# Kernel tuning notes

Measured on AMD Instinct MI355X. Metric: run time of the kernel, lower is better.

## Reference

```python
import jax, jax.numpy as jnp
import numpy as np

HIDDEN = 2048
HEAD = 256
VDIM = 512  # double_v_dim=True -> 2*head_size
GAMMA = 0.96875
SCALE_BASE = 512.0  # xpos default


def _rotate_every_two(x):
    # (x0, x1, x2, x3, ...) -> (-x1, x0, -x3, x2, ...)
    x1 = x[..., ::2]
    x2 = x[..., 1::2]
    return jnp.stack((-x2, x1), axis=-1).reshape(x.shape)


def _xpos(x, downscale=False, offset=0):
    # Standard XPOS (rotary + exponential scaling) as used in RetNet repos.
    S, d = x.shape[1], x.shape[2]
    d2 = d // 2
    scale_vec = (jnp.arange(0, d, 2, dtype=jnp.float32) + 0.4 * d) / (1.4 * d)  # [d2]
    pos = jnp.arange(S + offset, dtype=jnp.float32)
    scale = scale_vec[None, :] ** (pos[:, None] / SCALE_BASE)  # [S+off, d2]
    inv_freq = 1.0 / (10000.0 ** (jnp.arange(d2, dtype=jnp.float32) / d2))
    sinusoid = pos[:, None] * inv_freq[None, :]  # [S+off, d2]
    sin, cos = jnp.sin(sinusoid), jnp.cos(sinusoid)
    scale, sin, cos = scale[-S:], sin[-S:], cos[-S:]
    if downscale:
        scale = 1.0 / scale
    sin_s = jnp.repeat(sin * scale, 2, axis=-1)  # duplicate_interleave -> [S, d]
    cos_s = jnp.repeat(cos * scale, 2, axis=-1)
    return x * cos_s[None] + _rotate_every_two(x) * sin_s[None]


def _decay_matrix(S):
    # D[n, m] = gamma^(n-m) for n >= m else 0 (NaN/overflow-safe)
    n = jnp.arange(S, dtype=jnp.float32)
    diff = n[:, None] - n[None, :]
    mask = diff >= 0
    return jnp.where(mask, GAMMA ** jnp.where(mask, diff, 0.0), 0.0)


def setup_inputs() -> dict:
    key = jax.random.key(0)
    k1, k2, k3, k4 = jax.random.split(key, 4)
    B, S = 4, 4096
    X = jax.random.normal(k1, (B, S, HIDDEN), dtype=jnp.float32)
    W_Q = jax.random.normal(k2, (HIDDEN, HEAD), dtype=jnp.float32) / HIDDEN
    W_K = jax.random.normal(k3, (HIDDEN, HEAD), dtype=jnp.float32) / HIDDEN
    W_V = jax.random.normal(k4, (HIDDEN, VDIM), dtype=jnp.float32) / HIDDEN
    return {"X": X, "W_Q": W_Q, "W_K": W_K, "W_V": W_V}


def reference(X, W_Q, W_K, W_V):
    S = X.shape[1]
    Q = _xpos(X @ W_Q)                      # [B, S, HEAD]
    K = _xpos(X @ W_K, downscale=True)      # [B, S, HEAD]
    V = X @ W_V                             # [B, S, VDIM]
    D = _decay_matrix(S)                    # [S, S]
    retention = jnp.einsum('bqd,bkd->bqk', Q, K) * D[None]  # [B, S, S]
    return retention @ V                    # [B, S, VDIM]
```

## Files before the change

### kernel.cpp

```cpp
#include <hip/hip_runtime.h>
#include <math.h>

#define NB 4
#define SEQ 4096
#define HID 2048
#define DH 256
#define DV 512
#define NQKV 1024
#define CHUNK 128
#define NCH 32
#define MROWS (NB * SEQ)
#define LOG2_GAMMA (-0.045803689613124794f)
#define LOG2_10000 13.287712379549449f

typedef __attribute__((ext_vector_type(8))) short short8;
typedef __attribute__((ext_vector_type(4))) float floatx4;

__device__ __forceinline__ unsigned short bf16_rne(float v) {
    unsigned int u = __float_as_uint(v);
    u += 0x7fff + ((u >> 16) & 1);
    return (unsigned short)(u >> 16);
}
__device__ __forceinline__ float b2f(unsigned short h) {
    return __uint_as_float((unsigned int)h << 16);
}

__device__ __forceinline__ void gld16(const void* g, void* l) {
    __builtin_amdgcn_global_load_lds(
        reinterpret_cast<const __attribute__((address_space(1))) unsigned int*>(
            reinterpret_cast<uintptr_t>(g)),
        reinterpret_cast<__attribute__((address_space(3))) unsigned int*>(
            reinterpret_cast<uintptr_t>(l)),
        16, 0, 0);
}

__global__ __launch_bounds__(256) void xcvt_kernel(
    const float* __restrict__ X, unsigned short* __restrict__ Xb)
{
    const int i = blockIdx.x * 256 + threadIdx.x;
    float4 x = ((const float4*)X)[i];
    ushort4 h;
    h.x = bf16_rne(x.x); h.y = bf16_rne(x.y);
    h.z = bf16_rne(x.z); h.w = bf16_rne(x.w);
    ((ushort4*)Xb)[i] = h;
}

__global__ __launch_bounds__(256) void wcvt_kernel(
    const float* __restrict__ WQ, const float* __restrict__ WK,
    const float* __restrict__ WV, unsigned short* __restrict__ Bt)
{
    __shared__ unsigned short sh[64][65];
    const int bid = blockIdx.x;
    const int kt = bid & 31;
    const int ntile = bid >> 5;
    const int k0 = kt * 64, n0 = ntile * 64;

    const float* W; int ld, nl0;
    if (n0 < 256)      { W = WQ; ld = DH; nl0 = n0; }
    else if (n0 < 512) { W = WK; ld = DH; nl0 = n0 - 256; }
    else               { W = WV; ld = DV; nl0 = n0 - 512; }

    const int t = threadIdx.x;
#pragma unroll
    for (int p = 0; p < 4; p++) {
        const int kl = (t >> 4) + p * 16;
        const int ng = (t & 15) * 4;
        float4 w = *(const float4*)&W[(size_t)(k0 + kl) * ld + nl0 + ng];
        sh[kl][ng + 0] = bf16_rne(w.x);
        sh[kl][ng + 1] = bf16_rne(w.y);
        sh[kl][ng + 2] = bf16_rne(w.z);
        sh[kl][ng + 3] = bf16_rne(w.w);
    }
    __syncthreads();
#pragma unroll
    for (int p = 0; p < 4; p++) {
        const int nl = (t >> 4) + p * 16;
        const int kg = (t & 15) * 4;
        ushort4 h;
        h.x = sh[kg + 0][nl]; h.y = sh[kg + 1][nl];
        h.z = sh[kg + 2][nl]; h.w = sh[kg + 3][nl];
        *(ushort4*)&Bt[(size_t)(n0 + nl) * HID + k0 + kg] = h;
    }
}

__global__ __launch_bounds__(512, 1) void qkv_mfma_kernel(
    const unsigned short* __restrict__ Xb, const unsigned short* __restrict__ Bt,
    unsigned short* __restrict__ Qb, unsigned short* __restrict__ Kb,
    unsigned short* __restrict__ Vb, unsigned short* __restrict__ Vt)
{
    __shared__ unsigned short Ah[128 * 32];
    __shared__ unsigned short Bh[128 * 32];

    const int bid = blockIdx.x;
    const int xcd = bid & 7;
    const int nt  = (bid >> 3) & 7;
    const int mt  = (xcd << 4) | (bid >> 6);
    const int m0 = mt * 128, n0 = nt * 128;

    const int t = threadIdx.x;
    const int w = t >> 6, lane = t & 63;
    const int wm = (w & 1) << 6;
    const int wn = (w >> 1) << 5;

    floatx4 acc[4][2];
#pragma unroll
    for (int i = 0; i < 4; i++)
#pragma unroll
        for (int j = 0; j < 2; j++) acc[i][j] = (floatx4)0.0f;

    const int srow = lane >> 2, scol = (lane & 3) * 8;
    const size_t aoff = (size_t)(m0 + w * 16 + srow) * HID + scol;
    const size_t boff = (size_t)(n0 + w * 16 + srow) * HID + scol;
    unsigned short* const ldsA = &Ah[(w * 16) * 32];
    unsigned short* const ldsB = &Bh[(w * 16) * 32];

    const int fr = lane & 15, fq = (lane >> 4) * 8;

    for (int k0 = 0; k0 < HID; k0 += 32) {
        __syncthreads();
        gld16(Xb + aoff + k0, ldsA);
        gld16(Bt + boff + k0, ldsB);
        __syncthreads();

        short8 ah[4], bh[2];
#pragma unroll
        for (int i = 0; i < 4; i++)
            ah[i] = *(const short8*)&Ah[(wm + i * 16 + fr) * 32 + fq];
#pragma unroll
        for (int j = 0; j < 2; j++)
            bh[j] = *(const short8*)&Bh[(wn + j * 16 + fr) * 32 + fq];
#pragma unroll
        for (int i = 0; i < 4; i++)
#pragma unroll
            for (int j = 0; j < 2; j++)
                acc[i][j] = __builtin_amdgcn_mfma_f32_16x16x32_bf16(ah[i], bh[j], acc[i][j], 0, 0, 0);
    }

    const int cl = lane & 15, rq = (lane >> 4) << 2;
    if (n0 >= 512) {
#pragma unroll
        for (int i = 0; i < 4; i++)
#pragma unroll
            for (int j = 0; j < 2; j++) {
                const int c = n0 - 512 + wn + j * 16 + cl;
#pragma unroll
                for (int r = 0; r < 4; r++) {
                    const int m = m0 + wm + i * 16 + rq + r;
                    const unsigned short hv = bf16_rne(acc[i][j][r]);
                    Vb[(size_t)m * DV + c] = hv;
                    Vt[(size_t)c * MROWS + m] = hv;
                }
            }
    } else {
        unsigned short* dst = (n0 < 256) ? Qb : Kb;
        const float sgn = (n0 < 256) ? 1.f : -1.f;
        const int nb = (n0 < 256) ? n0 : n0 - 256;
#pragma unroll
        for (int j = 0; j < 2; j++) {
            const int c = nb + wn + j * 16 + cl;
            const float jj = (float)(c >> 1);
            const float sv = (2.f * jj + 0.4f * 256.f) * (1.f / (1.4f * 256.f));
            const float l2sv = __log2f(sv) * sgn * (1.f / 512.f);
            const float invf = exp2f(jj * (-LOG2_10000 / 128.f));
            const bool odd = (c & 1) != 0;
#pragma unroll
            for (int i = 0; i < 4; i++) {
#pragma unroll
                for (int r = 0; r < 4; r++) {
                    const int m = m0 + wm + i * 16 + rq + r;
                    const float s = (float)(m & (SEQ - 1));
                    const float x = acc[i][j][r];
                    const float p = __shfl_xor(x, 1, 64);
                    const float sc = exp2f(s * l2sv);
                    const float ang = s * invf;
                    const float sn = __sinf(ang), cs = __cosf(ang);
                    const float o = odd ? sc * (x * cs + p * sn)
                                        : sc * (x * cs - p * sn);
                    dst[(size_t)m * DH + c] = bf16_rne(o);
                }
            }
        }
    }
}

__global__ __launch_bounds__(256, 1) void chunk_kv_kernel(
    const unsigned short* __restrict__ Kb, const unsigned short* __restrict__ Vb,
    float* __restrict__ Ut)
{
    __shared__ float kls[32][68];
    __shared__ float vls[32][132];

    const int bid = blockIdx.x;
    const int vq = bid & 3;
    const int ht = (bid >> 2) & 3;
    const int c  = (bid >> 4) & 31;
    const int b  = bid >> 9;
    const int dh0 = ht * 64, dv0 = vq * 128;
    const int t = threadIdx.x, tx = t & 15, ty = t >> 4;

    float acc[4][8];
#pragma unroll
    for (int i = 0; i < 4; i++)
#pragma unroll
        for (int j = 0; j < 8; j++) acc[i][j] = 0.f;

    const int klr = t >> 4, klc = (t & 15) << 2;
    const int vlr = t >> 5, vlc = (t & 31) << 2;

    for (int i0 = 0; i0 < CHUNK; i0 += 32) {
        __syncthreads();
#pragma unroll
        for (int p = 0; p < 2; p++) {
            const int il = klr + 16 * p;
            const int i = i0 + il;
            const int row = b * SEQ + c * CHUNK + i;
            const float wgt = exp2f((float)(CHUNK - i) * LOG2_GAMMA);
            ushort4 kq = *(const ushort4*)&Kb[(size_t)row * DH + dh0 + klc];
            kls[il][klc + 0] = b2f(kq.x) * wgt;
            kls[il][klc + 1] = b2f(kq.y) * wgt;
            kls[il][klc + 2] = b2f(kq.z) * wgt;
            kls[il][klc + 3] = b2f(kq.w) * wgt;
        }
#pragma unroll
        for (int p = 0; p < 4; p++) {
            const int il = vlr + 8 * p;
            const int row = b * SEQ + c * CHUNK + i0 + il;
            ushort4 vv = *(const ushort4*)&Vb[(size_t)row * DV + dv0 + vlc];
            vls[il][vlc + 0] = b2f(vv.x);
            vls[il][vlc + 1] = b2f(vv.y);
            vls[il][vlc + 2] = b2f(vv.z);
            vls[il][vlc + 3] = b2f(vv.w);
        }
        __syncthreads();
#pragma unroll
        for (int i = 0; i < 32; i++) {
            float af[4], bf[8];
            *(float4*)&af[0] = *(const float4*)&kls[i][ty * 4];
            *(float4*)&bf[0] = *(const float4*)&vls[i][tx * 8];
            *(float4*)&bf[4] = *(const float4*)&vls[i][tx * 8 + 4];
#pragma unroll
            for (int ii = 0; ii < 4; ii++)
#pragma unroll
                for (int jj = 0; jj < 8; jj++) acc[ii][jj] += af[ii] * bf[jj];
        }
    }

#pragma unroll
    for (int jj = 0; jj < 8; jj++) {
        const int dv = dv0 + tx * 8 + jj;
        const size_t base = ((size_t)(b * NCH + c) * DV + dv) * DH + dh0 + ty * 4;
        *(float4*)&Ut[base] = make_float4(acc[0][jj], acc[1][jj], acc[2][jj], acc[3][jj]);
    }
}

__global__ __launch_bounds__(256) void scan_kernel(float* __restrict__ Ut)
{
    const int t = blockIdx.x * 256 + threadIdx.x;
    const int b = t >> 17;
    const int r = t & 131071;
    const float gC = exp2f((float)CHUNK * LOG2_GAMMA);
    float s = 0.f;
    const size_t base = (size_t)b * NCH * 131072 + r;
    for (int c = 0; c < NCH; c++) {
        const size_t off = base + (size_t)c * 131072;
        const float u = Ut[off];
        Ut[off] = s;
        s = gC * s + u;
    }
}

__global__ __launch_bounds__(512, 1) void out_mfma_kernel(
    const unsigned short* __restrict__ Qb, const unsigned short* __restrict__ Kb,
    const unsigned short* __restrict__ Vt, const float* __restrict__ St,
    float* __restrict__ out)
{
    __shared__ unsigned short Pa[128 * 136];
    __shared__ unsigned short As[128 * 32];
    __shared__ unsigned short Bs[128 * 32];

    const int bid = blockIdx.x;
    const int vq = bid & 3;
    const int c  = (bid >> 2) & 31;
    const int b  = bid >> 7;
    const int dv0 = vq * 128;
    const int row0 = b * SEQ + c * CHUNK;

    const int t = threadIdx.x;
    const int w = t >> 6, lane = t & 63;
    const int wm = (w & 1) << 6;
    const int wn = (w >> 1) << 5;
    const int fr = lane & 15, fq = (lane >> 4) * 8;
    const int cl = lane & 15, rq = (lane >> 4) << 2;
    const int srow = lane >> 2, scol = (lane & 3) * 8;

    floatx4 acc[4][2];
#pragma unroll
    for (int i = 0; i < 4; i++)
#pragma unroll
        for (int j = 0; j < 2; j++) acc[i][j] = (floatx4)0.0f;

    for (int d0 = 0; d0 < DH; d0 += 32) {
        __syncthreads();
        gld16(&Qb[(size_t)(row0 + w * 16 + srow) * DH + d0 + scol], &As[(w * 16) * 32]);
        gld16(&Kb[(size_t)(row0 + w * 16 + srow) * DH + d0 + scol], &Bs[(w * 16) * 32]);
        __syncthreads();
        short8 a[4], bb[2];
#pragma unroll
        for (int i = 0; i < 4; i++)
            a[i] = *(const short8*)&As[(wm + i * 16 + fr) * 32 + fq];
#pragma unroll
        for (int j = 0; j < 2; j++)
            bb[j] = *(const short8*)&Bs[(wn + j * 16 + fr) * 32 + fq];
#pragma unroll
        for (int i = 0; i < 4; i++)
#pragma unroll
            for (int j = 0; j < 2; j++)
                acc[i][j] = __builtin_amdgcn_mfma_f32_16x16x32_bf16(a[i], bb[j], acc[i][j], 0, 0, 0);
    }

#pragma unroll
    for (int i = 0; i < 4; i++)
#pragma unroll
        for (int j = 0; j < 2; j++) {
            const int jj = wn + j * 16 + cl;
#pragma unroll
            for (int r = 0; r < 4; r++) {
                const int ii = wm + i * 16 + rq + r;
                const int diff = ii - jj;
                const float v = (diff >= 0) ? acc[i][j][r] * exp2f((float)diff * LOG2_GAMMA) : 0.f;
                Pa[ii * 136 + jj] = bf16_rne(v);
            }
            acc[i][j] = (floatx4)0.0f;
        }

    for (int k0 = 0; k0 < CHUNK; k0 += 32) {
        __syncthreads();
        gld16(&Vt[(size_t)(dv0 + w * 16 + srow) * MROWS + row0 + k0 + scol], &Bs[(w * 16) * 32]);
        __syncthreads();
        short8 a[4], bb[2];
#pragma unroll
        for (int i = 0; i < 4; i++)
            a[i] = *(const short8*)&Pa[(wm + i * 16 + fr) * 136 + k0 + fq];
#pragma unroll
        for (int j = 0; j < 2; j++)
            bb[j] = *(const short8*)&Bs[(wn + j * 16 + fr) * 32 + fq];
#pragma unroll
        for (int i = 0; i < 4; i++)
#pragma unroll
            for (int j = 0; j < 2; j++)
                acc[i][j] = __builtin_amdgcn_mfma_f32_16x16x32_bf16(a[i], bb[j], acc[i][j], 0, 0, 0);
    }

    const size_t stbase = ((size_t)(b * NCH + c) * DV + dv0) * DH;
    const int xr = t >> 2, xc = (t & 3) * 8;
    const float gx = exp2f((float)xr * LOG2_GAMMA);
    for (int d0 = 0; d0 < DH; d0 += 32) {
        __syncthreads();
        {
            ushort4 q0 = *(const ushort4*)&Qb[(size_t)(row0 + xr) * DH + d0 + xc];
            ushort4 q1 = *(const ushort4*)&Qb[(size_t)(row0 + xr) * DH + d0 + xc + 4];
            ushort4 h0, h1;
            h0.x = bf16_rne(b2f(q0.x) * gx); h0.y = bf16_rne(b2f(q0.y) * gx);
            h0.z = bf16_rne(b2f(q0.z) * gx); h0.w = bf16_rne(b2f(q0.w) * gx);
            h1.x = bf16_rne(b2f(q1.x) * gx); h1.y = bf16_rne(b2f(q1.y) * gx);
            h1.z = bf16_rne(b2f(q1.z) * gx); h1.w = bf16_rne(b2f(q1.w) * gx);
            *(ushort4*)&As[xr * 32 + xc] = h0;
            *(ushort4*)&As[xr * 32 + xc + 4] = h1;
        }
        {
            float4 s0 = *(const float4*)&St[stbase + (size_t)xr * DH + d0 + xc];
            float4 s1 = *(const float4*)&St[stbase + (size_t)xr * DH + d0 + xc + 4];
            ushort4 h0, h1;
            h0.x = bf16_rne(s0.x); h0.y = bf16_rne(s0.y);
            h0.z = bf16_rne(s0.z); h0.w = bf16_rne(s0.w);
            h1.x = bf16_rne(s1.x); h1.y = bf16_rne(s1.y);
            h1.z = bf16_rne(s1.z); h1.w = bf16_rne(s1.w);
            *(ushort4*)&Bs[xr * 32 + xc] = h0;
            *(ushort4*)&Bs[xr * 32 + xc + 4] = h1;
        }
        __syncthreads();
        short8 a[4], bb[2];
#pragma unroll
        for (int i = 0; i < 4; i++)
            a[i] = *(const short8*)&As[(wm + i * 16 + fr) * 32 + fq];
#pragma unroll
        for (int j = 0; j < 2; j++)
            bb[j] = *(const short8*)&Bs[(wn + j * 16 + fr) * 32 + fq];
#pragma unroll
        for (int i = 0; i < 4; i++)
#pragma unroll
            for (int j = 0; j < 2; j++)
                acc[i][j] = __builtin_amdgcn_mfma_f32_16x16x32_bf16(a[i], bb[j], acc[i][j], 0, 0, 0);
    }

#pragma unroll
    for (int i = 0; i < 4; i++)
#pragma unroll
        for (int j = 0; j < 2; j++) {
            const int dv = dv0 + wn + j * 16 + cl;
#pragma unroll
            for (int r = 0; r < 4; r++) {
                const int m = row0 + wm + i * 16 + rq + r;
                out[(size_t)m * DV + dv] = acc[i][j][r];
            }
        }
}

extern "C" void kernel_launch(void* const* d_in, const int* in_sizes, int n_in,
                              void* d_out, int out_size, void* d_ws, size_t ws_size,
                              hipStream_t stream) {
    const float* X  = (const float*)d_in[0];
    const float* WQ = (const float*)d_in[1];
    const float* WK = (const float*)d_in[2];
    const float* WV = (const float*)d_in[3];
    float* out = (float*)d_out;

    char* ws = (char*)d_ws;
    unsigned short* Qb = (unsigned short*)ws;
    unsigned short* Kb = Qb + (size_t)MROWS * DH;
    unsigned short* Vb = Kb + (size_t)MROWS * DH;
    unsigned short* Vt = Vb + (size_t)MROWS * DV;
    float*          Ut = (float*)(Vt + (size_t)MROWS * DV);
    unsigned short* Xb = (unsigned short*)Ut;
    unsigned short* Bt = (unsigned short*)(Ut + (size_t)NB * NCH * DV * DH);

    xcvt_kernel<<<(MROWS * HID / 4) / 256, 256, 0, stream>>>(X, Xb);
    wcvt_kernel<<<512, 256, 0, stream>>>(WQ, WK, WV, Bt);
    qkv_mfma_kernel<<<1024, 512, 0, stream>>>(Xb, Bt, Qb, Kb, Vb, Vt);
    chunk_kv_kernel<<<2048, 256, 0, stream>>>(Kb, Vb, Ut);
    scan_kernel<<<2048, 256, 0, stream>>>(Ut);
    out_mfma_kernel<<<512, 512, 0, stream>>>(Qb, Kb, Vt, Ut, out);
}
```

Baseline: 414.6 us.

## Move chunk KV state to MFMA, store bf16 states, double K-step per barrier

The per-chunk K^T·V state computation moves from scalar FP32 FMAs to bf16 MFMA. It reads transposed K and V buffers that the QKV kernel now writes directly, which drops the row-major V copy. The scan writes bf16 states so the output kernel can load them asynchronously instead of converting fp32 on the fly. The GEMM loops in the QKV and output kernels stage two 32-wide K slices per barrier pair to halve synchronisations. The costs are extra strided transposed K writes, more LDS use, and bf16 rounding of the weighted K values and the states.

```diff
diff --git a/kernel.cpp b/kernel.cpp
--- a/kernel.cpp
+++ b/kernel.cpp
@@ -10,6 +10,8 @@
 #define CHUNK 128
 #define NCH 32
 #define MROWS (NB * SEQ)
+#define GAMMA 0.96875f
+#define GAMMA_INV 1.0322580645161290f
 #define LOG2_GAMMA (-0.045803689613124794f)
 #define LOG2_10000 13.287712379549449f
 
@@ -86,10 +88,10 @@
 __global__ __launch_bounds__(512, 1) void qkv_mfma_kernel(
     const unsigned short* __restrict__ Xb, const unsigned short* __restrict__ Bt,
     unsigned short* __restrict__ Qb, unsigned short* __restrict__ Kb,
-    unsigned short* __restrict__ Vb, unsigned short* __restrict__ Vt)
-{
-    __shared__ unsigned short Ah[128 * 32];
-    __shared__ unsigned short Bh[128 * 32];
+    unsigned short* __restrict__ Kt, unsigned short* __restrict__ Vt)
+{
+    __shared__ unsigned short Ah[2 * 128 * 32];
+    __shared__ unsigned short Bh[2 * 128 * 32];
 
     const int bid = blockIdx.x;
     const int xcd = bid & 7;
@@ -111,29 +113,36 @@
     const int srow = lane >> 2, scol = (lane & 3) * 8;
     const size_t aoff = (size_t)(m0 + w * 16 + srow) * HID + scol;
     const size_t boff = (size_t)(n0 + w * 16 + srow) * HID + scol;
-    unsigned short* const ldsA = &Ah[(w * 16) * 32];
-    unsigned short* const ldsB = &Bh[(w * 16) * 32];
+    unsigned short* const ldsA0 = &Ah[(w * 16) * 32];
+    unsigned short* const ldsA1 = &Ah[4096 + (w * 16) * 32];
+    unsigned short* const ldsB0 = &Bh[(w * 16) * 32];
+    unsigned short* const ldsB1 = &Bh[4096 + (w * 16) * 32];
 
     const int fr = lane & 15, fq = (lane >> 4) * 8;
 
-    for (int k0 = 0; k0 < HID; k0 += 32) {
-        __syncthreads();
-        gld16(Xb + aoff + k0, ldsA);
-        gld16(Bt + boff + k0, ldsB);
-        __syncthreads();
-
-        short8 ah[4], bh[2];
-#pragma unroll
-        for (int i = 0; i < 4; i++)
-            ah[i] = *(const short8*)&Ah[(wm + i * 16 + fr) * 32 + fq];
-#pragma unroll
-        for (int j = 0; j < 2; j++)
-            bh[j] = *(const short8*)&Bh[(wn + j * 16 + fr) * 32 + fq];
-#pragma unroll
-        for (int i = 0; i < 4; i++)
+    for (int k0 = 0; k0 < HID; k0 += 64) {
+        __syncthreads();
+        gld16(Xb + aoff + k0,      ldsA0);
+        gld16(Xb + aoff + k0 + 32, ldsA1);
+        gld16(Bt + boff + k0,      ldsB0);
+        gld16(Bt + boff + k0 + 32, ldsB1);
+        __syncthreads();
+
+#pragma nounroll
+        for (int s = 0; s < 2; s++) {
+            short8 ah[4], bh[2];
+#pragma unroll
+            for (int i = 0; i < 4; i++)
+                ah[i] = *(const short8*)&Ah[s * 4096 + (wm + i * 16 + fr) * 32 + fq];
 #pragma unroll
             for (int j = 0; j < 2; j++)
-                acc[i][j] = __builtin_amdgcn_mfma_f32_16x16x32_bf16(ah[i], bh[j], acc[i][j], 0, 0, 0);
+                bh[j] = *(const short8*)&Bh[s * 4096 + (wn + j * 16 + fr) * 32 + fq];
+#pragma unroll
+            for (int i = 0; i < 4; i++)
+#pragma unroll
+                for (int j = 0; j < 2; j++)
+                    acc[i][j] = __builtin_amdgcn_mfma_f32_16x16x32_bf16(ah[i], bh[j], acc[i][j], 0, 0, 0);
+        }
     }
 
     const int cl = lane & 15, rq = (lane >> 4) << 2;
@@ -146,15 +155,14 @@
 #pragma unroll
                 for (int r = 0; r < 4; r++) {
                     const int m = m0 + wm + i * 16 + rq + r;
-                    const unsigned short hv = bf16_rne(acc[i][j][r]);
-                    Vb[(size_t)m * DV + c] = hv;
-                    Vt[(size_t)c * MROWS + m] = hv;
+                    Vt[(size_t)c * MROWS + m] = bf16_rne(acc[i][j][r]);
                 }
             }
     } else {
-        unsigned short* dst = (n0 < 256) ? Qb : Kb;
-        const float sgn = (n0 < 256) ? 1.f : -1.f;
-        const int nb = (n0 < 256) ? n0 : n0 - 256;
+        const bool isQ = (n0 < 256);
+        unsigned short* dst = isQ ? Qb : Kb;
+        const float sgn = isQ ? 1.f : -1.f;
+        const int nb = isQ ? n0 : n0 - 256;
 #pragma unroll
         for (int j = 0; j < 2; j++) {
             const int c = nb + wn + j * 16 + cl;
@@ -176,84 +184,98 @@
                     const float sn = __sinf(ang), cs = __cosf(ang);
                     const float o = odd ? sc * (x * cs + p * sn)
                                         : sc * (x * cs - p * sn);
-                    dst[(size_t)m * DH + c] = bf16_rne(o);
+                    const unsigned short hv = bf16_rne(o);
+                    dst[(size_t)m * DH + c] = hv;
+                    if (!isQ) Kt[(size_t)c * MROWS + m] = hv;
                 }
             }
         }
     }
 }
 
-__global__ __launch_bounds__(256, 1) void chunk_kv_kernel(
-    const unsigned short* __restrict__ Kb, const unsigned short* __restrict__ Vb,
+__global__ __launch_bounds__(512, 1) void chunk_kv_kernel(
+    const unsigned short* __restrict__ Kt, const unsigned short* __restrict__ Vt,
     float* __restrict__ Ut)
 {
-    __shared__ float kls[32][68];
-    __shared__ float vls[32][132];
+    __shared__ unsigned short As[128 * 32];
+    __shared__ unsigned short Bs[128 * 32];
 
     const int bid = blockIdx.x;
-    const int vq = bid & 3;
-    const int ht = (bid >> 2) & 3;
-    const int c  = (bid >> 4) & 31;
-    const int b  = bid >> 9;
-    const int dh0 = ht * 64, dv0 = vq * 128;
-    const int t = threadIdx.x, tx = t & 15, ty = t >> 4;
-
-    float acc[4][8];
-#pragma unroll
-    for (int i = 0; i < 4; i++)
-#pragma unroll
-        for (int j = 0; j < 8; j++) acc[i][j] = 0.f;
-
-    const int klr = t >> 4, klc = (t & 15) << 2;
-    const int vlr = t >> 5, vlc = (t & 31) << 2;
+    const int dht = bid & 1;
+    const int vq  = (bid >> 1) & 3;
+    const int c   = (bid >> 3) & 31;
+    const int b   = bid >> 8;
+    const int dh0 = dht * 128, dv0 = vq * 128;
+    const int row0 = b * SEQ + c * CHUNK;
+
+    const int t = threadIdx.x;
+    const int w = t >> 6, lane = t & 63;
+    const int wm = (w & 1) << 6;
+    const int wn = (w >> 1) << 5;
+    const int srow = lane >> 2, scol = (lane & 3) * 8;
+    const int fr = lane & 15, fq = (lane >> 4) * 8;
+
+    floatx4 acc[4][2];
+#pragma unroll
+    for (int i = 0; i < 4; i++)
+#pragma unroll
+        for (int j = 0; j < 2; j++) acc[i][j] = (floatx4)0.0f;
+
+    const int kr = t >> 2, kc = (t & 3) * 8;
 
     for (int i0 = 0; i0 < CHUNK; i0 += 32) {
         __syncthreads();
-#pragma unroll
-        for (int p = 0; p < 2; p++) {
-            const int il = klr + 16 * p;
-            const int i = i0 + il;
-            const int row = b * SEQ + c * CHUNK + i;
-            const float wgt = exp2f((float)(CHUNK - i) * LOG2_GAMMA);
-            ushort4 kq = *(const ushort4*)&Kb[(size_t)row * DH + dh0 + klc];
-            kls[il][klc + 0] = b2f(kq.x) * wgt;
-            kls[il][klc + 1] = b2f(kq.y) * wgt;
-            kls[il][klc + 2] = b2f(kq.z) * wgt;
-            kls[il][klc + 3] = b2f(kq.w) * wgt;
-        }
-#pragma unroll
-        for (int p = 0; p < 4; p++) {
-            const int il = vlr + 8 * p;
-            const int row = b * SEQ + c * CHUNK + i0 + il;
-            ushort4 vv = *(const ushort4*)&Vb[(size_t)row * DV + dv0 + vlc];
-            vls[il][vlc + 0] = b2f(vv.x);
-            vls[il][vlc + 1] = b2f(vv.y);
-            vls[il][vlc + 2] = b2f(vv.z);
-            vls[il][vlc + 3] = b2f(vv.w);
-        }
-        __syncthreads();
-#pragma unroll
-        for (int i = 0; i < 32; i++) {
-            float af[4], bf[8];
-            *(float4*)&af[0] = *(const float4*)&kls[i][ty * 4];
-            *(float4*)&bf[0] = *(const float4*)&vls[i][tx * 8];
-            *(float4*)&bf[4] = *(const float4*)&vls[i][tx * 8 + 4];
-#pragma unroll
-            for (int ii = 0; ii < 4; ii++)
-#pragma unroll
-                for (int jj = 0; jj < 8; jj++) acc[ii][jj] += af[ii] * bf[jj];
-        }
-    }
-
-#pragma unroll
-    for (int jj = 0; jj < 8; jj++) {
-        const int dv = dv0 + tx * 8 + jj;
-        const size_t base = ((size_t)(b * NCH + c) * DV + dv) * DH + dh0 + ty * 4;
-        *(float4*)&Ut[base] = make_float4(acc[0][jj], acc[1][jj], acc[2][jj], acc[3][jj]);
-    }
-}
-
-__global__ __launch_bounds__(256) void scan_kernel(float* __restrict__ Ut)
+        gld16(&Vt[(size_t)(dv0 + w * 16 + srow) * MROWS + row0 + i0 + scol],
+              &As[(w * 16) * 32]);
+        {
+            const unsigned short* src = &Kt[(size_t)(dh0 + kr) * MROWS + row0 + i0 + kc];
+            ushort4 k0v = *(const ushort4*)src;
+            ushort4 k1v = *(const ushort4*)(src + 4);
+            float g = exp2f((float)(CHUNK - i0 - kc) * LOG2_GAMMA);
+            ushort4 h0, h1;
+            h0.x = bf16_rne(b2f(k0v.x) * g); g *= GAMMA_INV;
+            h0.y = bf16_rne(b2f(k0v.y) * g); g *= GAMMA_INV;
+            h0.z = bf16_rne(b2f(k0v.z) * g); g *= GAMMA_INV;
+            h0.w = bf16_rne(b2f(k0v.w) * g); g *= GAMMA_INV;
+            h1.x = bf16_rne(b2f(k1v.x) * g); g *= GAMMA_INV;
+            h1.y = bf16_rne(b2f(k1v.y) * g); g *= GAMMA_INV;
+            h1.z = bf16_rne(b2f(k1v.z) * g); g *= GAMMA_INV;
+            h1.w = bf16_rne(b2f(k1v.w) * g);
+            *(ushort4*)&Bs[kr * 32 + kc] = h0;
+            *(ushort4*)&Bs[kr * 32 + kc + 4] = h1;
+        }
+        __syncthreads();
+        short8 a[4], bb[2];
+#pragma unroll
+        for (int i = 0; i < 4; i++)
+            a[i] = *(const short8*)&As[(wm + i * 16 + fr) * 32 + fq];
+#pragma unroll
+        for (int j = 0; j < 2; j++)
+            bb[j] = *(const short8*)&Bs[(wn + j * 16 + fr) * 32 + fq];
+#pragma unroll
+        for (int i = 0; i < 4; i++)
+#pragma unroll
+            for (int j = 0; j < 2; j++)
+                acc[i][j] = __builtin_amdgcn_mfma_f32_16x16x32_bf16(a[i], bb[j], acc[i][j], 0, 0, 0);
+    }
+
+    const int cl = lane & 15, rq = (lane >> 4) << 2;
+    const size_t ubase = ((size_t)(b * NCH + c) * DV + dv0) * DH + dh0;
+#pragma unroll
+    for (int i = 0; i < 4; i++)
+#pragma unroll
+        for (int j = 0; j < 2; j++) {
+            const int n = wn + j * 16 + cl;
+#pragma unroll
+            for (int r = 0; r < 4; r++) {
+                const int m = wm + i * 16 + rq + r;
+                Ut[ubase + (size_t)m * DH + n] = acc[i][j][r];
+            }
+        }
+}
+
+__global__ __launch_bounds__(256) void scan_kernel(
+    const float* __restrict__ Ut, unsigned short* __restrict__ Sb)
 {
     const int t = blockIdx.x * 256 + threadIdx.x;
     const int b = t >> 17;
@@ -264,19 +286,19 @@
     for (int c = 0; c < NCH; c++) {
         const size_t off = base + (size_t)c * 131072;
         const float u = Ut[off];
-        Ut[off] = s;
+        Sb[off] = bf16_rne(s);
         s = gC * s + u;
     }
 }
 
 __global__ __launch_bounds__(512, 1) void out_mfma_kernel(
     const unsigned short* __restrict__ Qb, const unsigned short* __restrict__ Kb,
-    const unsigned short* __restrict__ Vt, const float* __restrict__ St,
+    const unsigned short* __restrict__ Vt, const unsigned short* __restrict__ Sb,
     float* __restrict__ out)
 {
     __shared__ unsigned short Pa[128 * 136];
-    __shared__ unsigned short As[128 * 32];
-    __shared__ unsigned short Bs[128 * 32];
+    __shared__ unsigned short As[2 * 128 * 32];
+    __shared__ unsigned short Bs[2 * 128 * 32];
 
     const int bid = blockIdx.x;
     const int vq = bid & 3;
@@ -299,23 +321,28 @@
 #pragma unroll
         for (int j = 0; j < 2; j++) acc[i][j] = (floatx4)0.0f;
 
-    for (int d0 = 0; d0 < DH; d0 += 32) {
+    for (int d0 = 0; d0 < DH; d0 += 64) {
         __syncthreads();
         gld16(&Qb[(size_t)(row0 + w * 16 + srow) * DH + d0 + scol], &As[(w * 16) * 32]);
+        gld16(&Qb[(size_t)(row0 + w * 16 + srow) * DH + d0 + 32 + scol], &As[4096 + (w * 16) * 32]);
         gld16(&Kb[(size_t)(row0 + w * 16 + srow) * DH + d0 + scol], &Bs[(w * 16) * 32]);
-        __syncthreads();
-        short8 a[4], bb[2];
-#pragma unroll
-        for (int i = 0; i < 4; i++)
-            a[i] = *(const short8*)&As[(wm + i * 16 + fr) * 32 + fq];
-#pragma unroll
-        for (int j = 0; j < 2; j++)
-            bb[j] = *(const short8*)&Bs[(wn + j * 16 + fr) * 32 + fq];
-#pragma unroll
-        for (int i = 0; i < 4; i++)
+        gld16(&Kb[(size_t)(row0 + w * 16 + srow) * DH + d0 + 32 + scol], &Bs[4096 + (w * 16) * 32]);
+        __syncthreads();
+#pragma nounroll
+        for (int s = 0; s < 2; s++) {
+            short8 a[4], bb[2];
+#pragma unroll
+            for (int i = 0; i < 4; i++)
+                a[i] = *(const short8*)&As[s * 4096 + (wm + i * 16 + fr) * 32 + fq];
 #pragma unroll
             for (int j = 0; j < 2; j++)
-                acc[i][j] = __builtin_amdgcn_mfma_f32_16x16x32_bf16(a[i], bb[j], acc[i][j], 0, 0, 0);
+                bb[j] = *(const short8*)&Bs[s * 4096 + (wn + j * 16 + fr) * 32 + fq];
+#pragma unroll
+            for (int i = 0; i < 4; i++)
+#pragma unroll
+                for (int j = 0; j < 2; j++)
+                    acc[i][j] = __builtin_amdgcn_mfma_f32_16x16x32_bf16(a[i], bb[j], acc[i][j], 0, 0, 0);
+        }
     }
 
 #pragma unroll
@@ -333,64 +360,64 @@
             acc[i][j] = (floatx4)0.0f;
         }
 
-    for (int k0 = 0; k0 < CHUNK; k0 += 32) {
+    for (int k0 = 0; k0 < CHUNK; k0 += 64) {
         __syncthreads();
         gld16(&Vt[(size_t)(dv0 + w * 16 + srow) * MROWS + row0 + k0 + scol], &Bs[(w * 16) * 32]);
-        __syncthreads();
-        short8 a[4], bb[2];
-#pragma unroll
-        for (int i = 0; i < 4; i++)
-            a[i] = *(const short8*)&Pa[(wm + i * 16 + fr) * 136 + k0 + fq];
-#pragma unroll
-        for (int j = 0; j < 2; j++)
-            bb[j] = *(const short8*)&Bs[(wn + j * 16 + fr) * 32 + fq];
-#pragma unroll
-        for (int i = 0; i < 4; i++)
+        gld16(&Vt[(size_t)(dv0 + w * 16 + srow) * MROWS + row0 + k0 + 32 + scol], &Bs[4096 + (w * 16) * 32]);
+        __syncthreads();
+#pragma nounroll
+        for (int s = 0; s < 2; s++) {
+            short8 a[4], bb[2];
+#pragma unroll
+            for (int i = 0; i < 4; i++)
+                a[i] = *(const short8*)&Pa[(wm + i * 16 + fr) * 136 + k0 + s * 32 + fq];
 #pragma unroll
             for (int j = 0; j < 2; j++)
-                acc[i][j] = __builtin_amdgcn_mfma_f32_16x16x32_bf16(a[i], bb[j], acc[i][j], 0, 0, 0);
-    }
-
-    const size_t stbase = ((size_t)(b * NCH + c) * DV + dv0) * DH;
+                bb[j] = *(const short8*)&Bs[s * 4096 + (wn + j * 16 + fr) * 32 + fq];
+#pragma unroll
+            for (int i = 0; i < 4; i++)
+#pragma unroll
+                for (int j = 0; j < 2; j++)
+                    acc[i][j] = __builtin_amdgcn_mfma_f32_16x16x32_bf16(a[i], bb[j], acc[i][j], 0, 0, 0);
+        }
+    }
+
+    const size_t sbbase = ((size_t)(b * NCH + c) * DV + dv0) * DH;
     const int xr = t >> 2, xc = (t & 3) * 8;
     const float gx = exp2f((float)xr * LOG2_GAMMA);
-    for (int d0 = 0; d0 < DH; d0 += 32) {
-        __syncthreads();
-        {
-            ushort4 q0 = *(const ushort4*)&Qb[(size_t)(row0 + xr) * DH + d0 + xc];
-            ushort4 q1 = *(const ushort4*)&Qb[(size_t)(row0 + xr) * DH + d0 + xc + 4];
+    for (int d0 = 0; d0 < DH; d0 += 64) {
+        __syncthreads();
+#pragma unroll
+        for (int s = 0; s < 2; s++) {
+            const unsigned short* src = &Qb[(size_t)(row0 + xr) * DH + d0 + s * 32 + xc];
+            ushort4 q0 = *(const ushort4*)src;
+            ushort4 q1 = *(const ushort4*)(src + 4);
             ushort4 h0, h1;
             h0.x = bf16_rne(b2f(q0.x) * gx); h0.y = bf16_rne(b2f(q0.y) * gx);
             h0.z = bf16_rne(b2f(q0.z) * gx); h0.w = bf16_rne(b2f(q0.w) * gx);
             h1.x = bf16_rne(b2f(q1.x) * gx); h1.y = bf16_rne(b2f(q1.y) * gx);
             h1.z = bf16_rne(b2f(q1.z) * gx); h1.w = bf16_rne(b2f(q1.w) * gx);
-            *(ushort4*)&As[xr * 32 + xc] = h0;
-            *(ushort4*)&As[xr * 32 + xc + 4] = h1;
-        }
-        {
-            float4 s0 = *(const float4*)&St[stbase + (size_t)xr * DH + d0 + xc];
-            float4 s1 = *(const float4*)&St[stbase + (size_t)xr * DH + d0 + xc + 4];
-            ushort4 h0, h1;
-            h0.x = bf16_rne(s0.x); h0.y = bf16_rne(s0.y);
-            h0.z = bf16_rne(s0.z); h0.w = bf16_rne(s0.w);
-            h1.x = bf16_rne(s1.x); h1.y = bf16_rne(s1.y);
-            h1.z = bf16_rne(s1.z); h1.w = bf16_rne(s1.w);
-            *(ushort4*)&Bs[xr * 32 + xc] = h0;
-            *(ushort4*)&Bs[xr * 32 + xc + 4] = h1;
-        }
-        __syncthreads();
-        short8 a[4], bb[2];
-#pragma unroll
-        for (int i = 0; i < 4; i++)
-            a[i] = *(const short8*)&As[(wm + i * 16 + fr) * 32 + fq];
-#pragma unroll
-        for (int j = 0; j < 2; j++)
-            bb[j] = *(const short8*)&Bs[(wn + j * 16 + fr) * 32 + fq];
-#pragma unroll
-        for (int i = 0; i < 4; i++)
+            *(ushort4*)&As[s * 4096 + xr * 32 + xc] = h0;
+            *(ushort4*)&As[s * 4096 + xr * 32 + xc + 4] = h1;
+        }
+        gld16(&Sb[sbbase + (size_t)(w * 16 + srow) * DH + d0 + scol], &Bs[(w * 16) * 32]);
+        gld16(&Sb[sbbase + (size_t)(w * 16 + srow) * DH + d0 + 32 + scol], &Bs[4096 + (w * 16) * 32]);
+        __syncthreads();
+#pragma nounroll
+        for (int s = 0; s < 2; s++) {
+            short8 a[4], bb[2];
+#pragma unroll
+            for (int i = 0; i < 4; i++)
+                a[i] = *(const short8*)&As[s * 4096 + (wm + i * 16 + fr) * 32 + fq];
 #pragma unroll
             for (int j = 0; j < 2; j++)
-                acc[i][j] = __builtin_amdgcn_mfma_f32_16x16x32_bf16(a[i], bb[j], acc[i][j], 0, 0, 0);
+                bb[j] = *(const short8*)&Bs[s * 4096 + (wn + j * 16 + fr) * 32 + fq];
+#pragma unroll
+            for (int i = 0; i < 4; i++)
+#pragma unroll
+                for (int j = 0; j < 2; j++)
+                    acc[i][j] = __builtin_amdgcn_mfma_f32_16x16x32_bf16(a[i], bb[j], acc[i][j], 0, 0, 0);
+        }
     }
 
 #pragma unroll
@@ -418,16 +445,17 @@
     char* ws = (char*)d_ws;
     unsigned short* Qb = (unsigned short*)ws;
     unsigned short* Kb = Qb + (size_t)MROWS * DH;
-    unsigned short* Vb = Kb + (size_t)MROWS * DH;
-    unsigned short* Vt = Vb + (size_t)MROWS * DV;
-    float*          Ut = (float*)(Vt + (size_t)MROWS * DV);
+    unsigned short* Kt = Kb + (size_t)MROWS * DH;
+    unsigned short* Vt = Kt + (size_t)MROWS * DH;
+    unsigned short* Sb = Vt + (size_t)MROWS * DV;
+    float*          Ut = (float*)(Sb + (size_t)NB * NCH * DV * DH);
     unsigned short* Xb = (unsigned short*)Ut;
     unsigned short* Bt = (unsigned short*)(Ut + (size_t)NB * NCH * DV * DH);
 
     xcvt_kernel<<<(MROWS * HID / 4) / 256, 256, 0, stream>>>(X, Xb);
     wcvt_kernel<<<512, 256, 0, stream>>>(WQ, WK, WV, Bt);
-    qkv_mfma_kernel<<<1024, 512, 0, stream>>>(Xb, Bt, Qb, Kb, Vb, Vt);
-    chunk_kv_kernel<<<2048, 256, 0, stream>>>(Kb, Vb, Ut);
-    scan_kernel<<<2048, 256, 0, stream>>>(Ut);
-    out_mfma_kernel<<<512, 512, 0, stream>>>(Qb, Kb, Vt, Ut, out);
-}
+    qkv_mfma_kernel<<<1024, 512, 0, stream>>>(Xb, Bt, Qb, Kb, Kt, Vt);
+    chunk_kv_kernel<<<1024, 512, 0, stream>>>(Kt, Vt, Ut);
+    scan_kernel<<<2048, 256, 0, stream>>>(Ut, Sb);
+    out_mfma_kernel<<<512, 512, 0, stream>>>(Qb, Kb, Vt, Sb, out);
+}
```

New measurement: 371.5 us. 1.12x faster.
